# Optimization experiments

Measured on AMD Instinct MI355X. Metric: run time of the kernel, lower is better.

The kernel has to match this reference:

```python
import jax, jax.numpy as jnp
import numpy as np

PH, PW, K = 32, 32, 2            # block grid and points per block
AROUND, AROUND_R, TOPK = 5, 0.1, 5
NHEAD = 8


def grid_sample(img, grid):
    # img [B,C,H,W]; grid [B,Hg,Wg,2], grid[...,0]=x (width), grid[...,1]=y (height)
    # torch defaults: bilinear, padding_mode='zeros', align_corners=False
    B, C, H, W = img.shape
    gx, gy = grid[..., 0], grid[..., 1]
    ix = ((gx + 1.0) * W - 1.0) * 0.5
    iy = ((gy + 1.0) * H - 1.0) * 0.5
    x0 = jnp.floor(ix)
    y0 = jnp.floor(iy)
    wx1 = ix - x0
    wy1 = iy - y0
    img_f = img.reshape(B, C, H * W)

    def gather(xf, yf):
        valid = (xf >= 0) & (xf <= W - 1) & (yf >= 0) & (yf <= H - 1)
        xi = jnp.clip(xf, 0, W - 1).astype(jnp.int32)
        yi = jnp.clip(yf, 0, H - 1).astype(jnp.int32)
        idx = (yi * W + xi).reshape(B, 1, -1)
        v = jnp.take_along_axis(img_f, jnp.broadcast_to(idx, (B, C, idx.shape[-1])), axis=2)
        v = v.reshape(B, C, *xf.shape[1:])
        return v * valid[:, None].astype(img.dtype)

    out = (gather(x0, y0) * ((1 - wx1) * (1 - wy1))[:, None]
           + gather(x0 + 1, y0) * (wx1 * (1 - wy1))[:, None]
           + gather(x0, y0 + 1) * ((1 - wx1) * wy1)[:, None]
           + gather(x0 + 1, y0 + 1) * (wx1 * wy1)[:, None])
    return out


def blockwise_sample(x, rand):
    # BlockwiseRandomSampler.forward (entirely under torch.no_grad)
    B = x.shape[0]
    bs = 2.0 / PH
    h0 = jnp.linspace(-1.0, 1.0 - bs, PH).reshape(1, PH, 1, 1)
    w0 = jnp.linspace(-1.0, 1.0 - bs, PW).reshape(1, 1, PW, 1)
    c0 = rand[..., 0] * bs + h0          # matches original: dim0 += h_starts
    c1 = rand[..., 1] * bs + w0
    coords = jnp.stack([c0, c1], -1).reshape(B, PH * PW * K, 2)
    pf = grid_sample(x, coords[:, None])[:, :, 0].transpose(0, 2, 1)  # [B,N,C]
    return jax.lax.stop_gradient(coords), jax.lax.stop_gradient(pf)


def soft_align(x1, pf, points, pos2d, arand):
    # pf [B,N,C], points [B,N,2]
    grid = points[:, None] + (arand * 2.0 - 0.5) * 2.0 * AROUND_R   # [B,A,N,2]
    grid = jax.lax.stop_gradient(jnp.clip(grid, -1.0, 1.0))
    emb = grid_sample(pos2d, grid)   # [B,C,A,N]
    af = grid_sample(x1, grid)       # [B,C,A,N]
    rep = jax.lax.stop_gradient(pf.transpose(0, 2, 1)[:, :, None])  # [B,C,1,N]
    num = jnp.sum(rep * af, axis=1)                                  # [B,A,N]
    den = jnp.maximum(jnp.linalg.norm(rep, axis=1), 1e-8) * jnp.maximum(jnp.linalg.norm(af, axis=1), 1e-8)
    w = jax.nn.softmax(num / den, axis=1)[:, None]                   # [B,1,A,N]
    return pf + jnp.sum(emb * w, axis=2).transpose(0, 2, 1)


def layer_norm(x, w, b):
    m = jnp.mean(x, -1, keepdims=True)
    v = jnp.mean((x - m) ** 2, -1, keepdims=True)
    return (x - m) / jnp.sqrt(v + 1e-5) * w + b


def mha(qx, kvx, in_w, in_b, out_w, out_b):
    B, Tq, C = qx.shape
    Tk = kvx.shape[1]
    hd = C // NHEAD
    q = (qx @ in_w[:, :C] + in_b[:C]).reshape(B, Tq, NHEAD, hd)
    k = (kvx @ in_w[:, C:2 * C] + in_b[C:2 * C]).reshape(B, Tk, NHEAD, hd)
    v = (kvx @ in_w[:, 2 * C:] + in_b[2 * C:]).reshape(B, Tk, NHEAD, hd)
    att = jax.nn.softmax(jnp.einsum('bqhd,bkhd->bhqk', q, k) * (1.0 / hd ** 0.5), axis=-1)
    o = jnp.einsum('bhqk,bkhd->bqhd', att, v).reshape(B, Tq, C)
    return o @ out_w + out_b


def _forward(mainx, others, position_embedding, modality_query, s_w1, s_b1, s_w2, s_b2,
             sa_in_w, sa_in_b, sa_out_w, sa_out_b, ca_in_w, ca_in_b, ca_out_w, ca_out_b,
             ff1_w, ff1_b, ff2_w, ff2_b, ln_w, ln_b, block_rand, around_rand):
    B, C, H, W = mainx.shape
    pos2d = jnp.broadcast_to(position_embedding.reshape(1, H, W, C).transpose(0, 3, 1, 2), (B, C, H, W))
    feats = []
    for i, x in enumerate(others):
        coords, pf = blockwise_sample(x, block_rand[i])
        score = jax.nn.sigmoid(jax.nn.relu(pf @ s_w1 + s_b1) @ s_w2 + s_b2)[..., 0]  # [B,N]
        idx = jax.lax.top_k(score, TOPK)[1]                                           # no_grad topk
        px = jnp.take_along_axis(coords, jnp.broadcast_to(idx[..., None], (B, TOPK, 2)), axis=1)
        pfk = jnp.take_along_axis(pf, jnp.broadcast_to(idx[..., None], (B, TOPK, C)), axis=1)
        apf = soft_align(mainx, pfk, px, pos2d, around_rand[i])
        feats.append(apf + modality_query[:, i + 1:i + 2])
    mem = jnp.concatenate(feats, axis=1)  # [B, M*TOPK, C]
    tgt = mainx.transpose(0, 2, 3, 1).reshape(B, H * W, C) + modality_query[:, 0:1] + position_embedding
    for l in range(sa_in_w.shape[0]):  # post-norm nn.TransformerDecoderLayer, relu, eval mode
        tgt = layer_norm(tgt + mha(tgt, tgt, sa_in_w[l], sa_in_b[l], sa_out_w[l], sa_out_b[l]), ln_w[l, 0], ln_b[l, 0])
        tgt = layer_norm(tgt + mha(tgt, mem, ca_in_w[l], ca_in_b[l], ca_out_w[l], ca_out_b[l]), ln_w[l, 1], ln_b[l, 1])
        tgt = layer_norm(tgt + (jax.nn.relu(tgt @ ff1_w[l] + ff1_b[l]) @ ff2_w[l] + ff2_b[l]), ln_w[l, 2], ln_b[l, 2])
    return tgt.reshape(B, H, W, C).transpose(0, 3, 1, 2)  # score_loss path is 0 (no gt/ps segments)


def setup_inputs():
    key = jax.random.key(0)
    ks = jax.random.split(key, 16)
    B, C, H, W, L, FF, M = 8, 768, 32, 32, 2, 3072, 2
    n = jax.random.normal
    d = {
        'mainx': n(ks[0], (B, C, H, W), jnp.float32),
        'other0': n(ks[1], (B, C, H, W), jnp.float32),
        'other1': n(ks[2], (B, C, H, W), jnp.float32),
        'position_embedding': 0.02 * n(ks[3], (1, H * W, C), jnp.float32),
        'modality_query': (0.02 * n(ks[4], (1, M + 1, C), jnp.float32)).at[:, 0].set(0.0),  # padding_idx=0
        's_w1': 0.02 * n(ks[5], (C, C), jnp.float32),
        's_b1': jnp.zeros((C,), jnp.float32),
        's_w2': 0.02 * n(ks[6], (C, 1), jnp.float32),
        's_b2': jnp.zeros((1,), jnp.float32),
        'sa_in_w': 0.02 * n(ks[7], (L, C, 3 * C), jnp.float32),
        'sa_in_b': jnp.zeros((L, 3 * C), jnp.float32),
        'sa_out_w': 0.02 * n(ks[8], (L, C, C), jnp.float32),
        'sa_out_b': jnp.zeros((L, C), jnp.float32),
        'ca_in_w': 0.02 * n(ks[9], (L, C, 3 * C), jnp.float32),
        'ca_in_b': jnp.zeros((L, 3 * C), jnp.float32),
        'ca_out_w': 0.02 * n(ks[10], (L, C, C), jnp.float32),
        'ca_out_b': jnp.zeros((L, C), jnp.float32),
        'ff1_w': 0.02 * n(ks[11], (L, C, FF), jnp.float32),
        'ff1_b': jnp.zeros((L, FF), jnp.float32),
        'ff2_w': 0.02 * n(ks[12], (L, FF, C), jnp.float32),
        'ff2_b': jnp.zeros((L, C), jnp.float32),
        'ln_w': jnp.ones((L, 3, C), jnp.float32),
        'ln_b': jnp.zeros((L, 3, C), jnp.float32),
        'block_rand': jax.random.uniform(ks[13], (M, B, PH, PW, K, 2), jnp.float32),
        'around_rand': jax.random.uniform(ks[14], (M, B, AROUND, TOPK, 2), jnp.float32),
    }
    return d


def reference(mainx, other0, other1, position_embedding, modality_query, s_w1, s_b1, s_w2, s_b2,
              sa_in_w, sa_in_b, sa_out_w, sa_out_b, ca_in_w, ca_in_b, ca_out_w, ca_out_b,
              ff1_w, ff1_b, ff2_w, ff2_b, ln_w, ln_b, block_rand, around_rand):
    return _forward(mainx, (other0, other1), position_embedding, modality_query, s_w1, s_b1, s_w2, s_b2,
                    sa_in_w, sa_in_b, sa_out_w, sa_out_b, ca_in_w, ca_in_b, ca_out_w, ca_out_b,
                    ff1_w, ff1_b, ff2_w, ff2_b, ln_w, ln_b, block_rand, around_rand)
```

## Files before the change

### kernel.cpp

```cpp
#include <hip/hip_runtime.h>
#include <hip/hip_bf16.h>
#include <math.h>

typedef __hip_bfloat16 hbf16;

#define B_ 8
#define C_ 768
#define HW_ 1024
#define NH_ 8
#define HD_ 96
#define NPTS 2048
#define AROUND_ 5
#define TOPK_ 5
#define MOD_ 2
#define FF_ 3072
#define TOK_ (B_*HW_)

typedef __attribute__((ext_vector_type(8))) short short8v;
typedef __attribute__((ext_vector_type(4))) short short4v;
typedef __attribute__((ext_vector_type(4))) float f32x4;

__device__ __forceinline__ float b2f(hbf16 v){ return __bfloat162float(v); }

__device__ __forceinline__ void gload16(const void* g, void* l) {
  __builtin_amdgcn_global_load_lds(
      (const __attribute__((address_space(1))) void*)g,
      (__attribute__((address_space(3))) void*)l, 16, 0, 0);
}

struct Taps { int x0,x1,y0,y1; float w00,w10,w01,w11; };
__device__ __forceinline__ Taps bilin_taps(float gx, float gy) {
  Taps t;
  float ix = ((gx+1.f)*32.f - 1.f)*0.5f;
  float iy = ((gy+1.f)*32.f - 1.f)*0.5f;
  float x0f = floorf(ix), y0f = floorf(iy);
  float wx1 = ix-x0f, wy1 = iy-y0f, wx0 = 1.f-wx1, wy0 = 1.f-wy1;
  int x0=(int)x0f, y0=(int)y0f, x1=x0+1, y1=y0+1;
  bool vx0=(x0>=0)&&(x0<=31), vx1=(x1>=0)&&(x1<=31);
  bool vy0=(y0>=0)&&(y0<=31), vy1=(y1>=0)&&(y1<=31);
  t.w00 = (vx0&&vy0) ? wx0*wy0 : 0.f;
  t.w10 = (vx1&&vy0) ? wx1*wy0 : 0.f;
  t.w01 = (vx0&&vy1) ? wx0*wy1 : 0.f;
  t.w11 = (vx1&&vy1) ? wx1*wy1 : 0.f;
  t.x0 = min(max(x0,0),31); t.x1 = min(max(x1,0),31);
  t.y0 = min(max(y0,0),31); t.y1 = min(max(y1,0),31);
  return t;
}

__device__ __forceinline__ float block_reduce_sum_256(float v, float* red) {
  int tid = threadIdx.x;
  red[tid] = v; __syncthreads();
  for (int s = 128; s > 0; s >>= 1) { if (tid < s) red[tid] += red[tid+s]; __syncthreads(); }
  float r = red[0]; __syncthreads();
  return r;
}

__global__ __launch_bounds__(256) void f2b_kernel(const float* __restrict__ in,
    hbf16* __restrict__ out, int n) {
  int i = (blockIdx.x*256 + threadIdx.x)*4;
  if (i >= n) return;
  float4 v = *(const float4*)&in[i];
  out[i+0] = __float2bfloat16(v.x);
  out[i+1] = __float2bfloat16(v.y);
  out[i+2] = __float2bfloat16(v.z);
  out[i+3] = __float2bfloat16(v.w);
}

__global__ __launch_bounds__(256) void wtrans_kernel(const float* __restrict__ in,
    hbf16* __restrict__ out, int K, int N) {
  __shared__ float t[32][33];
  int tx = threadIdx.x & 31, ty = threadIdx.x >> 5;
  int k0 = blockIdx.y*32, n0 = blockIdx.x*32;
  #pragma unroll
  for (int i = 0; i < 32; i += 8) t[ty+i][tx] = in[(size_t)(k0+ty+i)*N + n0+tx];
  __syncthreads();
  #pragma unroll
  for (int i = 0; i < 32; i += 8)
    out[(size_t)(n0+ty+i)*K + k0 + tx] = __float2bfloat16(t[tx][ty+i]);
}

__global__ __launch_bounds__(256) void wtrans_split_kernel(const float* __restrict__ in,
    hbf16* __restrict__ hi, hbf16* __restrict__ lo, int K, int N) {
  __shared__ float t[32][33];
  int tx = threadIdx.x & 31, ty = threadIdx.x >> 5;
  int k0 = blockIdx.y*32, n0 = blockIdx.x*32;
  #pragma unroll
  for (int i = 0; i < 32; i += 8) t[ty+i][tx] = in[(size_t)(k0+ty+i)*N + n0+tx];
  __syncthreads();
  #pragma unroll
  for (int i = 0; i < 32; i += 8) {
    float v = t[tx][ty+i];
    hbf16 h = __float2bfloat16(v);
    hi[(size_t)(n0+ty+i)*K + k0 + tx] = h;
    lo[(size_t)(n0+ty+i)*K + k0 + tx] = __float2bfloat16(v - b2f(h));
  }
}

__global__ __launch_bounds__(256) void btrans_kernel(const float* __restrict__ in,
    float* __restrict__ out, int R, int S) {
  __shared__ float t[32][33];
  int tx = threadIdx.x & 31, ty = threadIdx.x >> 5;
  int r0 = blockIdx.y*32, s0 = blockIdx.x*32;
  const float* ib = in + (size_t)blockIdx.z*R*S;
  float* ob = out + (size_t)blockIdx.z*R*S;
  #pragma unroll
  for (int i = 0; i < 32; i += 8) t[ty+i][tx] = ib[(size_t)(r0+ty+i)*S + s0+tx];
  __syncthreads();
  #pragma unroll
  for (int i = 0; i < 32; i += 8) ob[(size_t)(s0+ty+i)*R + r0+tx] = t[tx][ty+i];
}

__global__ __launch_bounds__(256) void zero_kernel(float* __restrict__ p, int n) {
  int i = blockIdx.x*256 + threadIdx.x;
  if (i < n) p[i] = 0.f;
}

__global__ __launch_bounds__(256) void sample_all_kernel(const float* __restrict__ oT,
    const float* __restrict__ brand, hbf16* __restrict__ pf_hi, hbf16* __restrict__ pf_lo,
    float* __restrict__ coords_all, int g0) {
  int ly = blockIdx.x;
  int inst = g0 + ly;
  int b = inst & 7;
  const float* xT = oT + (size_t)b*HW_*C_;
  int tid = threadIdx.x;
  int p = tid >> 6, lane = tid & 63;
  int n = blockIdx.y*4 + p;
  int k = n & 1, pw = (n >> 1) & 31, ph = n >> 6;
  const float* br = brand + (size_t)inst*4096;
  int roff = ((ph*32 + pw)*2 + k)*2;
  float r0 = br[roff], r1 = br[roff+1];
  const float bs = 0.0625f;
  float c0 = r0*bs + ((float)ph*bs - 1.0f);
  float c1 = r1*bs + ((float)pw*bs - 1.0f);
  Taps t = bilin_taps(c0, c1);
  const float* r00 = xT + (size_t)(t.y0*32+t.x0)*C_;
  const float* r10 = xT + (size_t)(t.y0*32+t.x1)*C_;
  const float* r01 = xT + (size_t)(t.y1*32+t.x0)*C_;
  const float* r11 = xT + (size_t)(t.y1*32+t.x1)*C_;
  size_t base = ((size_t)ly*NPTS + n)*C_;
  short* ph_ = (short*)pf_hi;
  short* pl_ = (short*)pf_lo;
  #pragma unroll
  for (int kk = 0; kk < 3; ++kk) {
    int c = kk*256 + lane*4;
    float4 v00 = *(const float4*)(r00 + c);
    float4 v10 = *(const float4*)(r10 + c);
    float4 v01 = *(const float4*)(r01 + c);
    float4 v11 = *(const float4*)(r11 + c);
    float o[4];
    o[0] = t.w00*v00.x + t.w10*v10.x + t.w01*v01.x + t.w11*v11.x;
    o[1] = t.w00*v00.y + t.w10*v10.y + t.w01*v01.y + t.w11*v11.y;
    o[2] = t.w00*v00.z + t.w10*v10.z + t.w01*v01.z + t.w11*v11.z;
    o[3] = t.w00*v00.w + t.w10*v10.w + t.w01*v01.w + t.w11*v11.w;
    short4v hs, ls;
    #pragma unroll
    for (int e = 0; e < 4; ++e) {
      hbf16 h = __float2bfloat16(o[e]);
      hs[e] = *(short*)&h;
      hbf16 l = __float2bfloat16(o[e] - b2f(h));
      ls[e] = *(short*)&l;
    }
    *(short4v*)&ph_[base + c] = hs;
    *(short4v*)&pl_[base + c] = ls;
  }
  if (lane == 0) {
    size_t co = ((size_t)inst*NPTS + n)*2;
    coords_all[co] = c0; coords_all[co+1] = c1;
  }
}

__device__ __forceinline__ void xcd_tile(int gx, int gy, int& row, int& col) {
  int wgid = blockIdx.y * gx + blockIdx.x;
  int xcd = wgid & 7;
  int li = wgid >> 3;
  row = xcd * (gy >> 3) + li / gx;
  col = li % gx;
}

__global__ __launch_bounds__(256) void score_gemm_kernel(const short* __restrict__ Ahi,
    const short* __restrict__ Alo, const short* __restrict__ Bhi, const short* __restrict__ Blo,
    const float* __restrict__ b1, const float* __restrict__ w2, float* __restrict__ logit) {
  __shared__ short AsH[128*32];
  __shared__ short AsL[128*32];
  __shared__ short BsH[128*32];
  __shared__ short BsL[128*32];
  int tid = threadIdx.x;
  int lane = tid & 63, w = tid >> 6;
  int wr = (w >> 1) * 64, wc = (w & 1) * 64;
  int m16 = lane & 15, quad = lane >> 4, q8 = quad * 8;
  int brow, bcol;
  xcd_tile(gridDim.x, gridDim.y, brow, bcol);
  int bm = brow * 128, bn = bcol * 128;
  int sr = w * 32;
  int lr = lane >> 2, lc = (lane & 3) * 8;
  f32x4 acc[4][4] = {};
  for (int k0 = 0; k0 < 768; k0 += 32) {
    {
      const short* pa = &Ahi[(size_t)(bm + sr + lr)*768 + k0 + lc];
      const short* pl = &Alo[(size_t)(bm + sr + lr)*768 + k0 + lc];
      const short* pb = &Bhi[(size_t)(bn + sr + lr)*768 + k0 + lc];
      const short* pq = &Blo[(size_t)(bn + sr + lr)*768 + k0 + lc];
      gload16(pa,            &AsH[sr*32]);
      gload16(pa + 16*768,   &AsH[(sr+16)*32]);
      gload16(pl,            &AsL[sr*32]);
      gload16(pl + 16*768,   &AsL[(sr+16)*32]);
      gload16(pb,            &BsH[sr*32]);
      gload16(pb + 16*768,   &BsH[(sr+16)*32]);
      gload16(pq,            &BsL[sr*32]);
      gload16(pq + 16*768,   &BsL[(sr+16)*32]);
    }
    __syncthreads();
    short8v ah[4], al[4], bh[4], bl[4];
    #pragma unroll
    for (int i=0;i<4;++i) {
      ah[i] = *(const short8v*)&AsH[(wr + i*16 + m16)*32 + q8];
      al[i] = *(const short8v*)&AsL[(wr + i*16 + m16)*32 + q8];
      bh[i] = *(const short8v*)&BsH[(wc + i*16 + m16)*32 + q8];
      bl[i] = *(const short8v*)&BsL[(wc + i*16 + m16)*32 + q8];
    }
    #pragma unroll
    for (int i=0;i<4;++i)
      #pragma unroll
      for (int j=0;j<4;++j) {
        acc[i][j] = __builtin_amdgcn_mfma_f32_16x16x32_bf16(ah[i], bh[j], acc[i][j], 0, 0, 0);
        acc[i][j] = __builtin_amdgcn_mfma_f32_16x16x32_bf16(ah[i], bl[j], acc[i][j], 0, 0, 0);
        acc[i][j] = __builtin_amdgcn_mfma_f32_16x16x32_bf16(al[i], bh[j], acc[i][j], 0, 0, 0);
      }
    __syncthreads();
  }
  float b1v[4], w2v[4];
  #pragma unroll
  for (int j=0;j<4;++j) {
    int col = bn + wc + j*16 + m16;
    b1v[j] = b1[col]; w2v[j] = w2[col];
  }
  #pragma unroll
  for (int i=0;i<4;++i) {
    #pragma unroll
    for (int r=0;r<4;++r) {
      float v = 0.f;
      #pragma unroll
      for (int j=0;j<4;++j) {
        float h = fmaxf(acc[i][j][r] + b1v[j], 0.f);
        v += h * w2v[j];
      }
      v += __shfl_xor(v, 1); v += __shfl_xor(v, 2);
      v += __shfl_xor(v, 4); v += __shfl_xor(v, 8);
      if (m16 == 0) atomicAdd(&logit[bm + wr + i*16 + quad*4 + r], v);
    }
  }
}

__global__ void topk_all_kernel(const float* __restrict__ logit, int* __restrict__ idx) {
  int lane = threadIdx.x;
  const float* score = logit + (size_t)blockIdx.x*NPTS;
  float v[32];
  #pragma unroll
  for (int i = 0; i < 32; ++i) v[i] = score[(i<<6) | lane];
  for (int t = 0; t < TOPK_; ++t) {
    float bv = v[0]; int bi = lane;
    #pragma unroll
    for (int i = 1; i < 32; ++i) { if (v[i] > bv) { bv = v[i]; bi = (i<<6)|lane; } }
    for (int off = 32; off; off >>= 1) {
      float ov = __shfl_xor(bv, off);
      int   oi = __shfl_xor(bi, off);
      if (ov > bv || (ov == bv && oi < bi)) { bv = ov; bi = oi; }
    }
    if (lane == 0) idx[blockIdx.x*8 + t] = bi;
    if ((bi & 63) == lane) v[bi >> 6] = -1e30f;
  }
}

__global__ __launch_bounds__(256) void softalign_all_kernel(const float* __restrict__ mainxT,
    const float* __restrict__ pos, const hbf16* __restrict__ pf_hi, const hbf16* __restrict__ pf_lo,
    const float* __restrict__ coords_all, const int* __restrict__ idx_all,
    const float* __restrict__ arand, const float* __restrict__ mq,
    float* __restrict__ memf, int g0) {
  int t = blockIdx.x;
  int ly = blockIdx.y;
  int inst = g0 + ly;
  int mod = inst >> 3, b = inst & 7;
  const float* mT_b = mainxT + (size_t)b*HW_*C_;
  const float* arand_ib = arand + (size_t)inst*AROUND_*TOPK_*2;
  const float* coords = coords_all + (size_t)inst*NPTS*2;
  int tid = threadIdx.x;
  int n = idx_all[ly*8 + t];
  float px0 = coords[n*2], px1 = coords[n*2+1];
  size_t pfb = ((size_t)ly*NPTS + n)*C_;
  float pfv[3];
  #pragma unroll
  for (int i=0;i<3;++i) {
    int c = tid + i*256;
    pfv[i] = b2f(pf_hi[pfb + c]) + b2f(pf_lo[pfb + c]);
  }
  __shared__ float red[256];
  float pp = block_reduce_sum_256(pfv[0]*pfv[0]+pfv[1]*pfv[1]+pfv[2]*pfv[2], red);
  float embr[AROUND_][3];
  float num_a[AROUND_], aa_a[AROUND_];
  for (int a=0; a<AROUND_; ++a) {
    int ar = (a*TOPK_ + t)*2;
    float g0c = px0 + (arand_ib[ar]*2.f - 0.5f)*0.2f;
    float g1c = px1 + (arand_ib[ar+1]*2.f - 0.5f)*0.2f;
    g0c = fminf(fmaxf(g0c,-1.f),1.f);
    g1c = fminf(fmaxf(g1c,-1.f),1.f);
    Taps tp = bilin_taps(g0c, g1c);
    int i00=tp.y0*32+tp.x0, i10=tp.y0*32+tp.x1, i01=tp.y1*32+tp.x0, i11=tp.y1*32+tp.x1;
    float s_num = 0.f, s_aa = 0.f;
    #pragma unroll
    for (int i=0;i<3;++i) {
      int c = tid + i*256;
      float af = tp.w00*mT_b[(size_t)i00*C_+c] + tp.w10*mT_b[(size_t)i10*C_+c]
               + tp.w01*mT_b[(size_t)i01*C_+c] + tp.w11*mT_b[(size_t)i11*C_+c];
      float em = tp.w00*pos[(size_t)i00*C_+c] + tp.w10*pos[(size_t)i10*C_+c]
               + tp.w01*pos[(size_t)i01*C_+c] + tp.w11*pos[(size_t)i11*C_+c];
      embr[a][i] = em;
      s_num += pfv[i]*af;
      s_aa  += af*af;
    }
    num_a[a] = block_reduce_sum_256(s_num, red);
    aa_a[a]  = block_reduce_sum_256(s_aa, red);
  }
  float pn = fmaxf(sqrtf(pp), 1e-8f);
  float w[AROUND_]; float mx = -1e30f;
  #pragma unroll
  for (int a=0;a<AROUND_;++a){ float den = pn * fmaxf(sqrtf(aa_a[a]),1e-8f); w[a]=num_a[a]/den; mx=fmaxf(mx,w[a]); }
  float se = 0.f;
  #pragma unroll
  for (int a=0;a<AROUND_;++a){ w[a]=expf(w[a]-mx); se+=w[a]; }
  float inv = 1.f/se;
  float* mo = memf + ((size_t)b*(MOD_*TOPK_) + mod*TOPK_ + t)*C_;
  #pragma unroll
  for (int i=0;i<3;++i) {
    int c = tid + i*256;
    float o = pfv[i];
    #pragma unroll
    for (int a=0;a<AROUND_;++a) o += embr[a][i]*(w[a]*inv);
    o += mq[(size_t)(mod+1)*C_ + c];
    mo[c] = o;
  }
}

#define BM 64
#define BN 64
#define BK 16
__global__ __launch_bounds__(256) void gemm_kernel(const float* __restrict__ A, int lda,
    const float* __restrict__ Bw, int ldb, const float* __restrict__ bias,
    float* __restrict__ Cm, int ldc, int M, int N, int K, int act) {
  __shared__ float As[BK][BM];
  __shared__ float Bs[BK][BN];
  int tid = threadIdx.x;
  int bm = blockIdx.y * BM, bn = blockIdx.x * BN;
  int arw = tid >> 2, acl = (tid & 3) << 2;
  int brw = tid >> 4, bcl = (tid & 15) << 2;
  int ty = tid >> 4, tx = tid & 15;
  float acc[4][4] = {{0.f}};
  for (int k0 = 0; k0 < K; k0 += BK) {
    float a0=0.f,a1=0.f,a2=0.f,a3=0.f;
    if (bm + arw < M) {
      const float* ap = A + (size_t)(bm+arw)*lda + k0 + acl;
      a0=ap[0]; a1=ap[1]; a2=ap[2]; a3=ap[3];
    }
    As[acl+0][arw]=a0; As[acl+1][arw]=a1; As[acl+2][arw]=a2; As[acl+3][arw]=a3;
    const float* bp = Bw + (size_t)(k0+brw)*ldb + bn + bcl;
    Bs[brw][bcl+0]=bp[0]; Bs[brw][bcl+1]=bp[1]; Bs[brw][bcl+2]=bp[2]; Bs[brw][bcl+3]=bp[3];
    __syncthreads();
    #pragma unroll
    for (int kk = 0; kk < BK; ++kk) {
      float4 av = *reinterpret_cast<const float4*>(&As[kk][ty<<2]);
      float4 bv = *reinterpret_cast<const float4*>(&Bs[kk][tx<<2]);
      acc[0][0]+=av.x*bv.x; acc[0][1]+=av.x*bv.y; acc[0][2]+=av.x*bv.z; acc[0][3]+=av.x*bv.w;
      acc[1][0]+=av.y*bv.x; acc[1][1]+=av.y*bv.y; acc[1][2]+=av.y*bv.z; acc[1][3]+=av.y*bv.w;
      acc[2][0]+=av.z*bv.x; acc[2][1]+=av.z*bv.y; acc[2][2]+=av.z*bv.z; acc[2][3]+=av.z*bv.w;
      acc[3][0]+=av.w*bv.x; acc[3][1]+=av.w*bv.y; acc[3][2]+=av.w*bv.z; acc[3][3]+=av.w*bv.w;
    }
    __syncthreads();
  }
  #pragma unroll
  for (int i=0;i<4;++i) {
    int r = bm + (ty<<2) + i;
    if (r >= M) continue;
    float* cp = Cm + (size_t)r*ldc + bn + (tx<<2);
    #pragma unroll
    for (int j=0;j<4;++j) {
      float v = acc[i][j] + bias[bn + (tx<<2) + j];
      if (act) v = fmaxf(v, 0.f);
      cp[j] = v;
    }
  }
}

__global__ __launch_bounds__(256) void gemm_mfma_t(const short* __restrict__ A, int lda,
    const short* __restrict__ Bt, int ldbt, const float* __restrict__ bias,
    hbf16* __restrict__ Cm, int ldc, int K, int act) {
  __shared__ short As[128*32];
  __shared__ short Bs[128*32];
  int tid = threadIdx.x;
  int lane = tid & 63, w = tid >> 6;
  int wr = (w >> 1) * 64, wc = (w & 1) * 64;
  int m16 = lane & 15, q8 = (lane >> 4) * 8;
  int brow, bcol;
  xcd_tile(gridDim.x, gridDim.y, brow, bcol);
  int bm = brow * 128, bn = bcol * 128;
  int sr = w * 32;
  int lr = lane >> 2, lc = (lane & 3) * 8;
  f32x4 acc[4][4] = {};
  for (int k0 = 0; k0 < K; k0 += 32) {
    {
      const short* pa = &A [(size_t)(bm + sr + lr)*lda  + k0 + lc];
      const short* pb = &Bt[(size_t)(bn + sr + lr)*ldbt + k0 + lc];
      gload16(pa,                    &As[sr*32]);
      gload16(pa + (size_t)16*lda,   &As[(sr+16)*32]);
      gload16(pb,                    &Bs[sr*32]);
      gload16(pb + (size_t)16*ldbt,  &Bs[(sr+16)*32]);
    }
    __syncthreads();
    short8v af[4], bf[4];
    #pragma unroll
    for (int i=0;i<4;++i) af[i] = *(const short8v*)&As[(wr + i*16 + m16)*32 + q8];
    #pragma unroll
    for (int j=0;j<4;++j) bf[j] = *(const short8v*)&Bs[(wc + j*16 + m16)*32 + q8];
    #pragma unroll
    for (int i=0;i<4;++i)
      #pragma unroll
      for (int j=0;j<4;++j)
        acc[i][j] = __builtin_amdgcn_mfma_f32_16x16x32_bf16(af[i], bf[j], acc[i][j], 0, 0, 0);
    __syncthreads();
  }
  #pragma unroll
  for (int j=0;j<4;++j) {
    int col = bn + wc + j*16 + m16;
    float bs = bias[col];
    #pragma unroll
    for (int i=0;i<4;++i) {
      int row0 = bm + wr + i*16 + (lane>>4)*4;
      #pragma unroll
      for (int r=0;r<4;++r) {
        float v = acc[i][j][r] + bs;
        if (act) v = fmaxf(v, 0.f);
        Cm[(size_t)(row0+r)*ldc + col] = __float2bfloat16(v);
      }
    }
  }
}

__global__ __launch_bounds__(256) void gemm_mfma_t64(const short* __restrict__ A, int lda,
    const short* __restrict__ Bt, int ldbt, const float* __restrict__ bias,
    hbf16* __restrict__ Cm, int ldc, int K, int act) {
  __shared__ short As[128*32];
  __shared__ short Bs[64*32];
  int tid = threadIdx.x;
  int lane = tid & 63, w = tid >> 6;
  int m16 = lane & 15, q8 = (lane >> 4) * 8;
  int brow, bcol;
  xcd_tile(gridDim.x, gridDim.y, brow, bcol);
  int bm = brow * 128, bn = bcol * 64;
  int sr = w * 32;
  int srB = w * 16;
  int lr = lane >> 2, lc = (lane & 3) * 8;
  f32x4 acc[2][4] = {};
  for (int k0 = 0; k0 < K; k0 += 32) {
    {
      const short* pa = &A [(size_t)(bm + sr  + lr)*lda  + k0 + lc];
      const short* pb = &Bt[(size_t)(bn + srB + lr)*ldbt + k0 + lc];
      gload16(pa,                   &As[sr*32]);
      gload16(pa + (size_t)16*lda,  &As[(sr+16)*32]);
      gload16(pb,                   &Bs[srB*32]);
    }
    __syncthreads();
    short8v af[2], bf[4];
    #pragma unroll
    for (int i=0;i<2;++i) af[i] = *(const short8v*)&As[(w*32 + i*16 + m16)*32 + q8];
    #pragma unroll
    for (int j=0;j<4;++j) bf[j] = *(const short8v*)&Bs[(j*16 + m16)*32 + q8];
    #pragma unroll
    for (int i=0;i<2;++i)
      #pragma unroll
      for (int j=0;j<4;++j)
        acc[i][j] = __builtin_amdgcn_mfma_f32_16x16x32_bf16(af[i], bf[j], acc[i][j], 0, 0, 0);
    __syncthreads();
  }
  #pragma unroll
  for (int j=0;j<4;++j) {
    int col = bn + j*16 + m16;
    float bs = bias[col];
    #pragma unroll
    for (int i=0;i<2;++i) {
      int row0 = bm + w*32 + i*16 + (lane>>4)*4;
      #pragma unroll
      for (int r=0;r<4;++r) {
        float v = acc[i][j][r] + bs;
        if (act) v = fmaxf(v, 0.f);
        Cm[(size_t)(row0+r)*ldc + col] = __float2bfloat16(v);
      }
    }
  }
}

__global__ __launch_bounds__(512, 4) void flash_attn_kernel(const hbf16* __restrict__ qkv_all,
    hbf16* __restrict__ o_all) {
  const int hb = blockIdx.x;
  const int h  = hb & 7;
  const int bz = hb >> 3;
  const int q0 = blockIdx.y * 128;
  const short* qkv = (const short*)(qkv_all + (size_t)bz*HW_*2304);
  hbf16* ob = o_all + (size_t)bz*HW_*C_;
  const int tid = threadIdx.x;
  const int lane = tid & 63, w = tid >> 6;
  const int m16 = lane & 15, quad = lane >> 4, q8 = quad * 8;
  const float scale = 0.10206207261596577f;

  __shared__ short lds[16128];
  short* KP = lds;
  short* Vt = lds + 9216;

  for (int idx = tid; idx < 128*12; idx += 512) {
    int row = idx / 12, dc = idx % 12;
    *(short8v*)&lds[row*104 + dc*8] = *(const short8v*)&qkv[(size_t)(q0+row)*2304 + h*HD_ + dc*8];
  }
  __syncthreads();
  short8v qf[3];
  #pragma unroll
  for (int kkk=0;kkk<3;++kkk)
    qf[kkk] = *(const short8v*)&lds[(w*16 + m16)*104 + q8 + kkk*32];
  __syncthreads();

  float m_st[4], l_st[4];
  f32x4 o_acc[6] = {};
  #pragma unroll
  for (int r=0;r<4;++r){ m_st[r] = -1e30f; l_st[r] = 0.f; }

  for (int t = 0; t < 16; ++t) {
    int j0 = t * 64;
    for (int idx = tid; idx < 64*12; idx += 512) {
      int row = idx / 12, dc = idx % 12;
      *(short8v*)&KP[row*104 + dc*8] = *(const short8v*)&qkv[(size_t)(j0+row)*2304 + C_ + h*HD_ + dc*8];
    }
    for (int idx = tid; idx < 64*12; idx += 512) {
      int j = idx & 63, dc = idx >> 6;
      short8v v = *(const short8v*)&qkv[(size_t)(j0+j)*2304 + 2*C_ + h*HD_ + dc*8];
      #pragma unroll
      for (int s = 0; s < 8; ++s) Vt[(dc*8+s)*72 + j] = v[s];
    }
    __syncthreads();

    f32x4 accs[4] = {};
    #pragma unroll
    for (int kkk = 0; kkk < 3; ++kkk) {
      int kk = kkk*32;
      short8v bf[4];
      #pragma unroll
      for (int n=0;n<4;++n) bf[n] = *(const short8v*)&KP[(n*16 + m16)*104 + q8 + kk];
      #pragma unroll
      for (int n=0;n<4;++n)
        accs[n] = __builtin_amdgcn_mfma_f32_16x16x32_bf16(qf[kkk], bf[n], accs[n], 0, 0, 0);
    }
    __syncthreads();

    #pragma unroll
    for (int r=0;r<4;++r) {
      float mx = -1e30f;
      #pragma unroll
      for (int n=0;n<4;++n) mx = fmaxf(mx, accs[n][r]*scale);
      #pragma unroll
      for (int off=1; off<16; off<<=1) mx = fmaxf(mx, __shfl_xor(mx, off));
      float m_new = fmaxf(m_st[r], mx);
      float alpha = __expf(m_st[r] - m_new);
      float psum = 0.f;
      int prow = (w*16 + quad*4 + r)*72 + m16;
      #pragma unroll
      for (int n=0;n<4;++n) {
        float pv = __expf(accs[n][r]*scale - m_new);
        psum += pv;
        *(hbf16*)&KP[prow + n*16] = __float2bfloat16(pv);
      }
      #pragma unroll
      for (int off=1; off<16; off<<=1) psum += __shfl_xor(psum, off);
      l_st[r] = l_st[r]*alpha + psum;
      m_st[r] = m_new;
      #pragma unroll
      for (int dt=0; dt<6; ++dt) o_acc[dt][r] *= alpha;
    }

    #pragma unroll
    for (int k0 = 0; k0 < 64; k0 += 32) {
      short8v pf_, vf[6];
      pf_ = *(const short8v*)&KP[(w*16 + m16)*72 + q8 + k0];
      #pragma unroll
      for (int dt=0; dt<6; ++dt) vf[dt] = *(const short8v*)&Vt[(dt*16 + m16)*72 + q8 + k0];
      #pragma unroll
      for (int dt=0; dt<6; ++dt)
        o_acc[dt] = __builtin_amdgcn_mfma_f32_16x16x32_bf16(pf_, vf[dt], o_acc[dt], 0, 0, 0);
    }
    __syncthreads();
  }

  #pragma unroll
  for (int r=0;r<4;++r) {
    float inv = 1.f / l_st[r];
    int row = q0 + w*16 + quad*4 + r;
    #pragma unroll
    for (int dt=0; dt<6; ++dt)
      ob[(size_t)row*C_ + h*HD_ + dt*16 + m16] = __float2bfloat16(o_acc[dt][r]*inv);
  }
}

__global__ __launch_bounds__(256) void cross_attn_kernel(hbf16* __restrict__ qb,
    const float* __restrict__ kvm, int b0) {
  int wv = threadIdx.x >> 6, lane = threadIdx.x & 63;
  int row = blockIdx.x*4 + wv;
  int lb = blockIdx.y;
  int b = b0 + lb;
  const float scale = 0.10206207261596577f;
  hbf16* qp = qb + ((size_t)lb*HW_ + row)*C_;
  int c0 = lane*12;
  const short* qs = (const short*)qp;
  float q[12];
  #pragma unroll
  for (int i0 = 0; i0 < 3; ++i0) {
    short4v s = *(const short4v*)&qs[c0 + i0*4];
    #pragma unroll
    for (int e = 0; e < 4; ++e) { hbf16 hh; *(short*)&hh = s[e]; q[i0*4+e] = b2f(hh); }
  }
  const float* kb = kvm + (size_t)(b*10)*1536;
  float sc[10];
  #pragma unroll
  for (int j = 0; j < 10; ++j) {
    const float* kp = kb + (size_t)j*1536 + c0;
    float4 k0 = *(const float4*)(kp);
    float4 k1 = *(const float4*)(kp+4);
    float4 k2 = *(const float4*)(kp+8);
    float s = q[0]*k0.x + q[1]*k0.y + q[2]*k0.z + q[3]*k0.w
            + q[4]*k1.x + q[5]*k1.y + q[6]*k1.z + q[7]*k1.w
            + q[8]*k2.x + q[9]*k2.y + q[10]*k2.z + q[11]*k2.w;
    s += __shfl_xor(s, 1); s += __shfl_xor(s, 2); s += __shfl_xor(s, 4);
    sc[j] = s * scale;
  }
  float m = sc[0];
  #pragma unroll
  for (int j=1;j<10;++j) m = fmaxf(m, sc[j]);
  float se = 0.f;
  #pragma unroll
  for (int j=0;j<10;++j){ sc[j] = __expf(sc[j]-m); se += sc[j]; }
  float inv = 1.f/se;
  float o[12] = {};
  #pragma unroll
  for (int j = 0; j < 10; ++j) {
    const float* vp = kb + (size_t)j*1536 + C_ + c0;
    float4 v0 = *(const float4*)(vp);
    float4 v1 = *(const float4*)(vp+4);
    float4 v2 = *(const float4*)(vp+8);
    float pj = sc[j]*inv;
    o[0]+=pj*v0.x; o[1]+=pj*v0.y; o[2]+=pj*v0.z; o[3]+=pj*v0.w;
    o[4]+=pj*v1.x; o[5]+=pj*v1.y; o[6]+=pj*v1.z; o[7]+=pj*v1.w;
    o[8]+=pj*v2.x; o[9]+=pj*v2.y; o[10]+=pj*v2.z; o[11]+=pj*v2.w;
  }
  short* qw = (short*)qp;
  #pragma unroll
  for (int i0 = 0; i0 < 3; ++i0) {
    short4v ov;
    #pragma unroll
    for (int e = 0; e < 4; ++e) { hbf16 hh = __float2bfloat16(o[i0*4+e]); ov[e] = *(short*)&hh; }
    *(short4v*)&qw[c0 + i0*4] = ov;
  }
}

__global__ __launch_bounds__(256) void tgt0_kernel(float* __restrict__ tgt,
    const float* __restrict__ mq, const float* __restrict__ pos) {
  size_t i = ((size_t)blockIdx.x*256 + threadIdx.x)*4;
  if (i >= (size_t)TOK_*C_) return;
  int c = (int)(i % C_);
  int tpos = (int)((i / C_) % HW_);
  float4 v = *(float4*)&tgt[i];
  float4 m = *(const float4*)&mq[c];
  float4 pp = *(const float4*)&pos[(size_t)tpos*C_ + c];
  v.x += m.x + pp.x; v.y += m.y + pp.y;
  v.z += m.z + pp.z; v.w += m.w + pp.w;
  *(float4*)&tgt[i] = v;
}

__global__ __launch_bounds__(256) void ln_res_kernel(float* __restrict__ tgt, const hbf16* __restrict__ add,
    const float* __restrict__ w, const float* __restrict__ bvec) {
  __shared__ float red[256];
  int row = blockIdx.x, tid = threadIdx.x;
  float* tp = tgt + (size_t)row*C_;
  const hbf16* ap = add + (size_t)row*C_;
  float x[3]; float s = 0.f, s2 = 0.f;
  #pragma unroll
  for (int i=0;i<3;++i){ int c=tid+i*256; float v=tp[c]+b2f(ap[c]); x[i]=v; s+=v; s2+=v*v; }
  s  = block_reduce_sum_256(s,  red);
  s2 = block_reduce_sum_256(s2, red);
  float mean = s * (1.f/C_);
  float var  = s2 * (1.f/C_) - mean*mean;
  float rstd = rsqrtf(var + 1e-5f);
  #pragma unroll
  for (int i=0;i<3;++i){ int c=tid+i*256; tp[c] = (x[i]-mean)*rstd*w[c] + bvec[c]; }
}

extern "C" void kernel_launch(void* const* d_in, const int* in_sizes, int n_in,
                              void* d_out, int out_size, void* d_ws, size_t ws_size,
                              hipStream_t stream) {
  const float* mainx   = (const float*)d_in[0];
  const float* other0  = (const float*)d_in[1];
  const float* other1  = (const float*)d_in[2];
  const float* pos     = (const float*)d_in[3];
  const float* mq      = (const float*)d_in[4];
  const float* s_w1    = (const float*)d_in[5];
  const float* s_b1    = (const float*)d_in[6];
  const float* s_w2    = (const float*)d_in[7];
  const float* sa_in_w = (const float*)d_in[9];
  const float* sa_in_b = (const float*)d_in[10];
  const float* sa_out_w= (const float*)d_in[11];
  const float* sa_out_b= (const float*)d_in[12];
  const float* ca_in_w = (const float*)d_in[13];
  const float* ca_in_b = (const float*)d_in[14];
  const float* ca_out_w= (const float*)d_in[15];
  const float* ca_out_b= (const float*)d_in[16];
  const float* ff1_w   = (const float*)d_in[17];
  const float* ff1_b   = (const float*)d_in[18];
  const float* ff2_w   = (const float*)d_in[19];
  const float* ff2_b   = (const float*)d_in[20];
  const float* ln_w    = (const float*)d_in[21];
  const float* ln_b    = (const float*)d_in[22];
  const float* brand   = (const float*)d_in[23];
  const float* arand   = (const float*)d_in[24];

  char* p = (char*)d_ws;
  auto alloc = [&](size_t bytes) { char* r = p; p += (bytes + 255) & ~(size_t)255; return (void*)r; };
  float* tgt    = (float*)alloc((size_t)TOK_*C_*4);
  hbf16* wb0    = (hbf16*)alloc((size_t)2359296*2);
  hbf16* wb1    = (hbf16*)alloc((size_t)2359296*2);
  hbf16* w1t_hi = (hbf16*)alloc((size_t)C_*C_*2);
  hbf16* w1t_lo = (hbf16*)alloc((size_t)C_*C_*2);
  float* kvm    = (float*)alloc((size_t)80*1536*4);
  float* memf   = (float*)alloc((size_t)80*C_*4);
  float* coords = (float*)alloc((size_t)16*NPTS*2*4);
  float* logit  = (float*)alloc((size_t)16*NPTS*4);
  int*   idxb   = (int*)alloc(16*8*4);
  char*  S      = p;
  size_t used = (size_t)(p - (char*)d_ws);
  size_t Savail = (ws_size > used) ? ws_size - used : 0;
  int CH = 1;
  if (Savail >= (size_t)8*1024*9216 + 4096) CH = 8;
  else if (Savail >= (size_t)4*1024*9216 + 4096) CH = 4;
  else if (Savail >= (size_t)2*1024*9216 + 4096) CH = 2;
  const size_t R = (size_t)CH*1024;
  const size_t perG = (size_t)NPTS*C_*2*2;
  const size_t oTb = (size_t)B_*HW_*C_*4;
  float* oT = (float*)S;
  char* Spf = S + oTb;
  size_t SA = (Savail > oTb) ? Savail - oTb : 0;
  int G = 1;
  if (SA >= 8*perG) G = 8;
  else if (SA >= 4*perG) G = 4;
  else if (SA >= 2*perG) G = 2;

  btrans_kernel<<<dim3(HW_/32, C_/32, B_), 256, 0, stream>>>(mainx, tgt, C_, HW_);
  wtrans_split_kernel<<<dim3(C_/32, C_/32), 256, 0, stream>>>(s_w1, w1t_hi, w1t_lo, C_, C_);
  zero_kernel<<<16*NPTS/256, 256, 0, stream>>>(logit, 16*NPTS);
  for (int g0 = 0; g0 < 16; g0 += G) {
    if ((g0 & 7) == 0)
      btrans_kernel<<<dim3(HW_/32, C_/32, B_), 256, 0, stream>>>(g0 < 8 ? other0 : other1,
          oT, C_, HW_);
    hbf16* pf_hi = (hbf16*)Spf;
    hbf16* pf_lo = pf_hi + (size_t)G*NPTS*C_;
    sample_all_kernel<<<dim3(G, NPTS/4), 256, 0, stream>>>(oT, brand,
        pf_hi, pf_lo, coords, g0);
    score_gemm_kernel<<<dim3(6, G*16), 256, 0, stream>>>((const short*)pf_hi, (const short*)pf_lo,
        (const short*)w1t_hi, (const short*)w1t_lo, s_b1, s_w2, logit + (size_t)g0*NPTS);
    topk_all_kernel<<<G, 64, 0, stream>>>(logit + (size_t)g0*NPTS, idxb + g0*8);
    softalign_all_kernel<<<dim3(TOPK_, G), 256, 0, stream>>>(tgt, pos, pf_hi, pf_lo,
        coords, idxb + g0*8, arand, mq, memf, g0);
  }

  size_t total = (size_t)TOK_*C_;
  tgt0_kernel<<<(int)((total/4+255)/256), 256, 0, stream>>>(tgt, mq, pos);

  for (int l = 0; l < 2; ++l) {
    wtrans_kernel<<<dim3(3*C_/32, C_/32), 256, 0, stream>>>(sa_in_w + (size_t)l*C_*3*C_, wb0, C_, 3*C_);
    wtrans_kernel<<<dim3(C_/32, C_/32), 256, 0, stream>>>(sa_out_w + (size_t)l*C_*C_, wb1, C_, C_);
    for (int c0 = 0; c0 < B_; c0 += CH) {
      float* tgtc = tgt + (size_t)c0*HW_*C_;
      hbf16* abuf = (hbf16*)S;
      hbf16* qkv  = abuf + R*C_;
      hbf16* oatt = qkv + R*3*C_;
      hbf16* tmpb = oatt + R*C_;
      f2b_kernel<<<(int)((R*C_/4+255)/256), 256, 0, stream>>>(tgtc, abuf, (int)(R*C_));
      gemm_mfma_t<<<dim3(3*C_/128, (int)(R/128)), 256, 0, stream>>>((const short*)abuf, C_,
          (const short*)wb0, C_, sa_in_b + (size_t)l*3*C_, qkv, 3*C_, C_, 0);
      flash_attn_kernel<<<dim3(NH_*CH, HW_/128), 512, 0, stream>>>(qkv, oatt);
      gemm_mfma_t64<<<dim3(C_/64, (int)(R/128)), 256, 0, stream>>>((const short*)oatt, C_,
          (const short*)wb1, C_, sa_out_b + (size_t)l*C_, tmpb, C_, C_, 0);
      ln_res_kernel<<<(int)R, 256, 0, stream>>>(tgtc, tmpb,
          ln_w + (size_t)(l*3+0)*C_, ln_b + (size_t)(l*3+0)*C_);
    }

    wtrans_kernel<<<dim3(C_/32, C_/32), 256, 0, stream>>>(ca_in_w + (size_t)l*C_*3*C_, wb0, C_, 3*C_);
    wtrans_kernel<<<dim3(C_/32, C_/32), 256, 0, stream>>>(ca_out_w + (size_t)l*C_*C_, wb1, C_, C_);
    gemm_kernel<<<dim3((2*C_+BN-1)/BN, (80+BM-1)/BM), 256, 0, stream>>>(memf, C_,
        ca_in_w + (size_t)l*C_*3*C_ + C_, 3*C_, ca_in_b + (size_t)l*3*C_ + C_, kvm, 2*C_,
        80, 2*C_, C_, 0);
    for (int c0 = 0; c0 < B_; c0 += CH) {
      float* tgtc = tgt + (size_t)c0*HW_*C_;
      hbf16* abuf = (hbf16*)S;
      hbf16* qb   = abuf + R*C_;
      hbf16* tmpb = qb + R*C_;
      f2b_kernel<<<(int)((R*C_/4+255)/256), 256, 0, stream>>>(tgtc, abuf, (int)(R*C_));
      gemm_mfma_t64<<<dim3(C_/64, (int)(R/128)), 256, 0, stream>>>((const short*)abuf, C_,
          (const short*)wb0, C_, ca_in_b + (size_t)l*3*C_, qb, C_, C_, 0);
      cross_attn_kernel<<<dim3(HW_/4, CH), 256, 0, stream>>>(qb, kvm, c0);
      gemm_mfma_t64<<<dim3(C_/64, (int)(R/128)), 256, 0, stream>>>((const short*)qb, C_,
          (const short*)wb1, C_, ca_out_b + (size_t)l*C_, tmpb, C_, C_, 0);
      ln_res_kernel<<<(int)R, 256, 0, stream>>>(tgtc, tmpb,
          ln_w + (size_t)(l*3+1)*C_, ln_b + (size_t)(l*3+1)*C_);
    }

    wtrans_kernel<<<dim3(FF_/32, C_/32), 256, 0, stream>>>(ff1_w + (size_t)l*C_*FF_, wb0, C_, FF_);
    wtrans_kernel<<<dim3(C_/32, FF_/32), 256, 0, stream>>>(ff2_w + (size_t)l*FF_*C_, wb1, FF_, C_);
    for (int c0 = 0; c0 < B_; c0 += CH) {
      float* tgtc = tgt + (size_t)c0*HW_*C_;
      hbf16* abuf = (hbf16*)S;
      hbf16* ffh  = abuf + R*C_;
      hbf16* tmpb = ffh + R*FF_;
      f2b_kernel<<<(int)((R*C_/4+255)/256), 256, 0, stream>>>(tgtc, abuf, (int)(R*C_));
      gemm_mfma_t<<<dim3(FF_/128, (int)(R/128)), 256, 0, stream>>>((const short*)abuf, C_,
          (const short*)wb0, C_, ff1_b + (size_t)l*FF_, ffh, FF_, C_, 1);
      gemm_mfma_t64<<<dim3(C_/64, (int)(R/128)), 256, 0, stream>>>((const short*)ffh, FF_,
          (const short*)wb1, FF_, ff2_b + (size_t)l*C_, tmpb, C_, FF_, 0);
      ln_res_kernel<<<(int)R, 256, 0, stream>>>(tgtc, tmpb,
          ln_w + (size_t)(l*3+2)*C_, ln_b + (size_t)(l*3+2)*C_);
    }
  }

  btrans_kernel<<<dim3(C_/32, HW_/32, B_), 256, 0, stream>>>(tgt, (float*)d_out, HW_, C_);
}
```

Measured before the change: 1.388 ms.

## Double-buffer K/V tiles in flash attention and fuse bf16 casts into layernorm

The flash attention kernel now double-buffers K and V tiles in shared memory. It prefetches the next tile into registers while the current tile's MFMAs run, raises wave priority around the MFMA sections, and drops one barrier per iteration. Separately, the standalone float-to-bf16 conversion kernels are removed: tgt0 and ln_res now also write a persistent bf16 copy of the activations, which the following GEMMs read directly. This adds shared memory per block, which may lower occupancy, and a workspace buffer of the full token size.

```diff
diff --git a/kernel.cpp b/kernel.cpp
--- a/kernel.cpp
+++ b/kernel.cpp
@@ -53,17 +53,6 @@
   for (int s = 128; s > 0; s >>= 1) { if (tid < s) red[tid] += red[tid+s]; __syncthreads(); }
   float r = red[0]; __syncthreads();
   return r;
-}
-
-__global__ __launch_bounds__(256) void f2b_kernel(const float* __restrict__ in,
-    hbf16* __restrict__ out, int n) {
-  int i = (blockIdx.x*256 + threadIdx.x)*4;
-  if (i >= n) return;
-  float4 v = *(const float4*)&in[i];
-  out[i+0] = __float2bfloat16(v.x);
-  out[i+1] = __float2bfloat16(v.y);
-  out[i+2] = __float2bfloat16(v.z);
-  out[i+3] = __float2bfloat16(v.w);
 }
 
 __global__ __launch_bounds__(256) void wtrans_kernel(const float* __restrict__ in,
@@ -509,9 +498,8 @@
   const int m16 = lane & 15, quad = lane >> 4, q8 = quad * 8;
   const float scale = 0.10206207261596577f;
 
-  __shared__ short lds[16128];
-  short* KP = lds;
-  short* Vt = lds + 9216;
+  __shared__ short lds[36352];
+  short* P = lds + 27136;
 
   for (int idx = tid; idx < 128*12; idx += 512) {
     int row = idx / 12, dc = idx % 12;
@@ -524,37 +512,55 @@
     qf[kkk] = *(const short8v*)&lds[(w*16 + m16)*104 + q8 + kkk*32];
   __syncthreads();
 
+  for (int idx = tid; idx < 768; idx += 512) {
+    int row = idx / 12, dc = idx % 12;
+    *(short8v*)&lds[row*104 + dc*8] = *(const short8v*)&qkv[(size_t)row*2304 + C_ + h*HD_ + dc*8];
+    int j = idx & 63, dcv = idx >> 6;
+    short8v v = *(const short8v*)&qkv[(size_t)j*2304 + 2*C_ + h*HD_ + dcv*8];
+    #pragma unroll
+    for (int s = 0; s < 8; ++s) lds[13312 + (dcv*8+s)*72 + j] = v[s];
+  }
+  __syncthreads();
+
   float m_st[4], l_st[4];
   f32x4 o_acc[6] = {};
   #pragma unroll
   for (int r=0;r<4;++r){ m_st[r] = -1e30f; l_st[r] = 0.f; }
 
   for (int t = 0; t < 16; ++t) {
-    int j0 = t * 64;
-    for (int idx = tid; idx < 64*12; idx += 512) {
-      int row = idx / 12, dc = idx % 12;
-      *(short8v*)&KP[row*104 + dc*8] = *(const short8v*)&qkv[(size_t)(j0+row)*2304 + C_ + h*HD_ + dc*8];
-    }
-    for (int idx = tid; idx < 64*12; idx += 512) {
-      int j = idx & 63, dc = idx >> 6;
-      short8v v = *(const short8v*)&qkv[(size_t)(j0+j)*2304 + 2*C_ + h*HD_ + dc*8];
-      #pragma unroll
-      for (int s = 0; s < 8; ++s) Vt[(dc*8+s)*72 + j] = v[s];
-    }
-    __syncthreads();
+    int cur = t & 1;
+    short* Kc = lds + (cur ? 6656 : 0);
+    short* Vc = lds + (cur ? 20224 : 13312);
+
+    short8v kr0, kr1, vr0, vr1;
+    if (t < 15) {
+      int j0n = (t+1)*64;
+      { int row = tid/12, dc = tid%12;
+        kr0 = *(const short8v*)&qkv[(size_t)(j0n+row)*2304 + C_ + h*HD_ + dc*8];
+        int j = tid & 63, dcv = tid >> 6;
+        vr0 = *(const short8v*)&qkv[(size_t)(j0n+j)*2304 + 2*C_ + h*HD_ + dcv*8]; }
+      if (tid < 256) {
+        int idx = tid + 512;
+        int row = idx/12, dc = idx%12;
+        kr1 = *(const short8v*)&qkv[(size_t)(j0n+row)*2304 + C_ + h*HD_ + dc*8];
+        int j = idx & 63, dcv = idx >> 6;
+        vr1 = *(const short8v*)&qkv[(size_t)(j0n+j)*2304 + 2*C_ + h*HD_ + dcv*8];
+      }
+    }
 
     f32x4 accs[4] = {};
+    __builtin_amdgcn_s_setprio(1);
     #pragma unroll
     for (int kkk = 0; kkk < 3; ++kkk) {
       int kk = kkk*32;
       short8v bf[4];
       #pragma unroll
-      for (int n=0;n<4;++n) bf[n] = *(const short8v*)&KP[(n*16 + m16)*104 + q8 + kk];
+      for (int n=0;n<4;++n) bf[n] = *(const short8v*)&Kc[(n*16 + m16)*104 + q8 + kk];
       #pragma unroll
       for (int n=0;n<4;++n)
         accs[n] = __builtin_amdgcn_mfma_f32_16x16x32_bf16(qf[kkk], bf[n], accs[n], 0, 0, 0);
     }
-    __syncthreads();
+    __builtin_amdgcn_s_setprio(0);
 
     #pragma unroll
     for (int r=0;r<4;++r) {
@@ -571,7 +577,7 @@
       for (int n=0;n<4;++n) {
         float pv = __expf(accs[n][r]*scale - m_new);
         psum += pv;
-        *(hbf16*)&KP[prow + n*16] = __float2bfloat16(pv);
+        *(hbf16*)&P[prow + n*16] = __float2bfloat16(pv);
       }
       #pragma unroll
       for (int off=1; off<16; off<<=1) psum += __shfl_xor(psum, off);
@@ -581,15 +587,35 @@
       for (int dt=0; dt<6; ++dt) o_acc[dt][r] *= alpha;
     }
 
+    __builtin_amdgcn_s_setprio(1);
     #pragma unroll
     for (int k0 = 0; k0 < 64; k0 += 32) {
       short8v pf_, vf[6];
-      pf_ = *(const short8v*)&KP[(w*16 + m16)*72 + q8 + k0];
-      #pragma unroll
-      for (int dt=0; dt<6; ++dt) vf[dt] = *(const short8v*)&Vt[(dt*16 + m16)*72 + q8 + k0];
+      pf_ = *(const short8v*)&P[(w*16 + m16)*72 + q8 + k0];
+      #pragma unroll
+      for (int dt=0; dt<6; ++dt) vf[dt] = *(const short8v*)&Vc[(dt*16 + m16)*72 + q8 + k0];
       #pragma unroll
       for (int dt=0; dt<6; ++dt)
         o_acc[dt] = __builtin_amdgcn_mfma_f32_16x16x32_bf16(pf_, vf[dt], o_acc[dt], 0, 0, 0);
+    }
+    __builtin_amdgcn_s_setprio(0);
+
+    if (t < 15) {
+      short* Kn = lds + (cur ? 0 : 6656);
+      short* Vn = lds + (cur ? 13312 : 20224);
+      { int row = tid/12, dc = tid%12;
+        *(short8v*)&Kn[row*104 + dc*8] = kr0;
+        int j = tid & 63, dcv = tid >> 6;
+        #pragma unroll
+        for (int s = 0; s < 8; ++s) Vn[(dcv*8+s)*72 + j] = vr0[s]; }
+      if (tid < 256) {
+        int idx = tid + 512;
+        int row = idx/12, dc = idx%12;
+        *(short8v*)&Kn[row*104 + dc*8] = kr1;
+        int j = idx & 63, dcv = idx >> 6;
+        #pragma unroll
+        for (int s = 0; s < 8; ++s) Vn[(dcv*8+s)*72 + j] = vr1[s];
+      }
     }
     __syncthreads();
   }
@@ -665,7 +691,7 @@
 }
 
 __global__ __launch_bounds__(256) void tgt0_kernel(float* __restrict__ tgt,
-    const float* __restrict__ mq, const float* __restrict__ pos) {
+    const float* __restrict__ mq, const float* __restrict__ pos, hbf16* __restrict__ outb) {
   size_t i = ((size_t)blockIdx.x*256 + threadIdx.x)*4;
   if (i >= (size_t)TOK_*C_) return;
   int c = (int)(i % C_);
@@ -676,14 +702,21 @@
   v.x += m.x + pp.x; v.y += m.y + pp.y;
   v.z += m.z + pp.z; v.w += m.w + pp.w;
   *(float4*)&tgt[i] = v;
+  short4v ov;
+  hbf16 h0 = __float2bfloat16(v.x); ov[0] = *(short*)&h0;
+  hbf16 h1 = __float2bfloat16(v.y); ov[1] = *(short*)&h1;
+  hbf16 h2 = __float2bfloat16(v.z); ov[2] = *(short*)&h2;
+  hbf16 h3 = __float2bfloat16(v.w); ov[3] = *(short*)&h3;
+  *(short4v*)&((short*)outb)[i] = ov;
 }
 
 __global__ __launch_bounds__(256) void ln_res_kernel(float* __restrict__ tgt, const hbf16* __restrict__ add,
-    const float* __restrict__ w, const float* __restrict__ bvec) {
+    const float* __restrict__ w, const float* __restrict__ bvec, hbf16* __restrict__ outb) {
   __shared__ float red[256];
   int row = blockIdx.x, tid = threadIdx.x;
   float* tp = tgt + (size_t)row*C_;
   const hbf16* ap = add + (size_t)row*C_;
+  hbf16* op = outb + (size_t)row*C_;
   float x[3]; float s = 0.f, s2 = 0.f;
   #pragma unroll
   for (int i=0;i<3;++i){ int c=tid+i*256; float v=tp[c]+b2f(ap[c]); x[i]=v; s+=v; s2+=v*v; }
@@ -693,7 +726,12 @@
   float var  = s2 * (1.f/C_) - mean*mean;
   float rstd = rsqrtf(var + 1e-5f);
   #pragma unroll
-  for (int i=0;i<3;++i){ int c=tid+i*256; tp[c] = (x[i]-mean)*rstd*w[c] + bvec[c]; }
+  for (int i=0;i<3;++i){
+    int c=tid+i*256;
+    float y = (x[i]-mean)*rstd*w[c] + bvec[c];
+    tp[c] = y;
+    op[c] = __float2bfloat16(y);
+  }
 }
 
 extern "C" void kernel_launch(void* const* d_in, const int* in_sizes, int n_in,
@@ -727,6 +765,7 @@
   char* p = (char*)d_ws;
   auto alloc = [&](size_t bytes) { char* r = p; p += (bytes + 255) & ~(size_t)255; return (void*)r; };
   float* tgt    = (float*)alloc((size_t)TOK_*C_*4);
+  hbf16* tgt_bf = (hbf16*)alloc((size_t)TOK_*C_*2);
   hbf16* wb0    = (hbf16*)alloc((size_t)2359296*2);
   hbf16* wb1    = (hbf16*)alloc((size_t)2359296*2);
   hbf16* w1t_hi = (hbf16*)alloc((size_t)C_*C_*2);
@@ -740,9 +779,9 @@
   size_t used = (size_t)(p - (char*)d_ws);
   size_t Savail = (ws_size > used) ? ws_size - used : 0;
   int CH = 1;
-  if (Savail >= (size_t)8*1024*9216 + 4096) CH = 8;
-  else if (Savail >= (size_t)4*1024*9216 + 4096) CH = 4;
-  else if (Savail >= (size_t)2*1024*9216 + 4096) CH = 2;
+  if (Savail >= (size_t)8*1024*7680 + 4096) CH = 8;
+  else if (Savail >= (size_t)4*1024*7680 + 4096) CH = 4;
+  else if (Savail >= (size_t)2*1024*7680 + 4096) CH = 2;
   const size_t R = (size_t)CH*1024;
   const size_t perG = (size_t)NPTS*C_*2*2;
   const size_t oTb = (size_t)B_*HW_*C_*4;
@@ -773,25 +812,24 @@
   }
 
   size_t total = (size_t)TOK_*C_;
-  tgt0_kernel<<<(int)((total/4+255)/256), 256, 0, stream>>>(tgt, mq, pos);
+  tgt0_kernel<<<(int)((total/4+255)/256), 256, 0, stream>>>(tgt, mq, pos, tgt_bf);
 
   for (int l = 0; l < 2; ++l) {
     wtrans_kernel<<<dim3(3*C_/32, C_/32), 256, 0, stream>>>(sa_in_w + (size_t)l*C_*3*C_, wb0, C_, 3*C_);
     wtrans_kernel<<<dim3(C_/32, C_/32), 256, 0, stream>>>(sa_out_w + (size_t)l*C_*C_, wb1, C_, C_);
     for (int c0 = 0; c0 < B_; c0 += CH) {
       float* tgtc = tgt + (size_t)c0*HW_*C_;
-      hbf16* abuf = (hbf16*)S;
-      hbf16* qkv  = abuf + R*C_;
+      hbf16* abuf = tgt_bf + (size_t)c0*HW_*C_;
+      hbf16* qkv  = (hbf16*)S;
       hbf16* oatt = qkv + R*3*C_;
       hbf16* tmpb = oatt + R*C_;
-      f2b_kernel<<<(int)((R*C_/4+255)/256), 256, 0, stream>>>(tgtc, abuf, (int)(R*C_));
       gemm_mfma_t<<<dim3(3*C_/128, (int)(R/128)), 256, 0, stream>>>((const short*)abuf, C_,
           (const short*)wb0, C_, sa_in_b + (size_t)l*3*C_, qkv, 3*C_, C_, 0);
       flash_attn_kernel<<<dim3(NH_*CH, HW_/128), 512, 0, stream>>>(qkv, oatt);
       gemm_mfma_t64<<<dim3(C_/64, (int)(R/128)), 256, 0, stream>>>((const short*)oatt, C_,
           (const short*)wb1, C_, sa_out_b + (size_t)l*C_, tmpb, C_, C_, 0);
       ln_res_kernel<<<(int)R, 256, 0, stream>>>(tgtc, tmpb,
-          ln_w + (size_t)(l*3+0)*C_, ln_b + (size_t)(l*3+0)*C_);
+          ln_w + (size_t)(l*3+0)*C_, ln_b + (size_t)(l*3+0)*C_, abuf);
     }
 
     wtrans_kernel<<<dim3(C_/32, C_/32), 256, 0, stream>>>(ca_in_w + (size_t)l*C_*3*C_, wb0, C_, 3*C_);
@@ -801,33 +839,31 @@
         80, 2*C_, C_, 0);
     for (int c0 = 0; c0 < B_; c0 += CH) {
       float* tgtc = tgt + (size_t)c0*HW_*C_;
-      hbf16* abuf = (hbf16*)S;
-      hbf16* qb   = abuf + R*C_;
+      hbf16* abuf = tgt_bf + (size_t)c0*HW_*C_;
+      hbf16* qb   = (hbf16*)S;
       hbf16* tmpb = qb + R*C_;
-      f2b_kernel<<<(int)((R*C_/4+255)/256), 256, 0, stream>>>(tgtc, abuf, (int)(R*C_));
       gemm_mfma_t64<<<dim3(C_/64, (int)(R/128)), 256, 0, stream>>>((const short*)abuf, C_,
           (const short*)wb0, C_, ca_in_b + (size_t)l*3*C_, qb, C_, C_, 0);
       cross_attn_kernel<<<dim3(HW_/4, CH), 256, 0, stream>>>(qb, kvm, c0);
       gemm_mfma_t64<<<dim3(C_/64, (int)(R/128)), 256, 0, stream>>>((const short*)qb, C_,
           (const short*)wb1, C_, ca_out_b + (size_t)l*C_, tmpb, C_, C_, 0);
       ln_res_kernel<<<(int)R, 256, 0, stream>>>(tgtc, tmpb,
-          ln_w + (size_t)(l*3+1)*C_, ln_b + (size_t)(l*3+1)*C_);
+          ln_w + (size_t)(l*3+1)*C_, ln_b + (size_t)(l*3+1)*C_, abuf);
     }
 
     wtrans_kernel<<<dim3(FF_/32, C_/32), 256, 0, stream>>>(ff1_w + (size_t)l*C_*FF_, wb0, C_, FF_);
     wtrans_kernel<<<dim3(C_/32, FF_/32), 256, 0, stream>>>(ff2_w + (size_t)l*FF_*C_, wb1, FF_, C_);
     for (int c0 = 0; c0 < B_; c0 += CH) {
       float* tgtc = tgt + (size_t)c0*HW_*C_;
-      hbf16* abuf = (hbf16*)S;
-      hbf16* ffh  = abuf + R*C_;
+      hbf16* abuf = tgt_bf + (size_t)c0*HW_*C_;
+      hbf16* ffh  = (hbf16*)S;
       hbf16* tmpb = ffh + R*FF_;
-      f2b_kernel<<<(int)((R*C_/4+255)/256), 256, 0, stream>>>(tgtc, abuf, (int)(R*C_));
       gemm_mfma_t<<<dim3(FF_/128, (int)(R/128)), 256, 0, stream>>>((const short*)abuf, C_,
           (const short*)wb0, C_, ff1_b + (size_t)l*FF_, ffh, FF_, C_, 1);
       gemm_mfma_t64<<<dim3(C_/64, (int)(R/128)), 256, 0, stream>>>((const short*)ffh, FF_,
           (const short*)wb1, FF_, ff2_b + (size_t)l*C_, tmpb, C_, FF_, 0);
       ln_res_kernel<<<(int)R, 256, 0, stream>>>(tgtc, tmpb,
-          ln_w + (size_t)(l*3+2)*C_, ln_b + (size_t)(l*3+2)*C_);
+          ln_w + (size_t)(l*3+2)*C_, ln_b + (size_t)(l*3+2)*C_, abuf);
     }
   }
 
```

After: 1.319 ms. -5.0%, faster.
